# Optimization experiments

Hardware: AMD Instinct MI355X
Metric: run time of the kernel (lower is better)

## Reference

```python
import jax, jax.numpy as jnp
import numpy as np

B, S, E, H, NQ, FF = 4, 1024, 256, 32, 8, 1024
DK = E // H  # 8, equals n_wires of the quantum attention layer
EPS = 1e-5


def layernorm(x, g, b):
    mu = jnp.mean(x, axis=-1, keepdims=True)
    var = jnp.mean(jnp.square(x - mu), axis=-1, keepdims=True)
    return (x - mu) * jax.lax.rsqrt(var + EPS) * g + b


def setup_inputs() -> dict:
    key = jax.random.key(0)
    ks = jax.random.split(key, 20)
    s = lambda n: 1.0 / np.sqrt(n)
    return {
        "x": jax.random.normal(ks[0], (B, S, E), dtype=jnp.float32),
        # quantum attention trainable RX angles (one per wire)
        "theta_attn": jax.random.uniform(ks[1], (DK,), minval=-np.pi, maxval=np.pi),
        # nn.MultiheadAttention packed in-proj and out-proj
        "w_in": jax.random.normal(ks[2], (3 * E, E)) * s(E),
        "b_in": jnp.zeros((3 * E,), jnp.float32),
        "w_out": jax.random.normal(ks[3], (E, E)) * s(E),
        "b_out": jnp.zeros((E,), jnp.float32),
        # combine linear
        "w_comb": jax.random.normal(ks[4], (E, E)) * s(E),
        "b_comb": jnp.zeros((E,), jnp.float32),
        # layernorms
        "g1": jnp.ones((E,), jnp.float32), "be1": jnp.zeros((E,), jnp.float32),
        "g2": jnp.ones((E,), jnp.float32), "be2": jnp.zeros((E,), jnp.float32),
        # FFN: input_proj, quantum RY angles, linear1, linear2
        "w_ip": jax.random.normal(ks[5], (NQ, E)) * s(E),
        "b_ip": jnp.zeros((NQ,), jnp.float32),
        "theta_ffn": jax.random.uniform(ks[6], (NQ,), minval=-np.pi, maxval=np.pi),
        "w1": jax.random.normal(ks[7], (FF, NQ)) * s(NQ),
        "b1": jnp.zeros((FF,), jnp.float32),
        "w2": jax.random.normal(ks[8], (E, FF)) * s(FF),
        "b2": jnp.zeros((E,), jnp.float32),
    }


def reference(x, theta_attn, w_in, b_in, w_out, b_out, w_comb, b_comb,
              g1, be1, g2, be2, w_ip, b_ip, theta_ffn, w1, b1, w2, b2):
    batch, seq, embed = x.shape
    # ---- QuantumAttention ----
    # per-head RX(x_i) encoding followed by trainable RX(theta_i): <Z_i> = cos(x_i + theta_i)
    xh = x.reshape(batch, seq, H, DK)            # [B,S,H,dk]
    q_out = jnp.cos(xh + theta_attn).reshape(batch, seq, embed)
    # standard multi-head self-attention on q_out (q=k=v)
    qkv = q_out @ w_in.T + b_in                  # [B,S,3E]
    q, k, v = jnp.split(qkv, 3, axis=-1)
    def heads(t):
        return t.reshape(batch, seq, H, DK).transpose(0, 2, 1, 3)  # [B,H,S,dk]
    q, k, v = heads(q), heads(k), heads(v)
    scores = jnp.einsum('bhqd,bhkd->bhqk', q, k) / np.sqrt(DK)
    attn = jax.nn.softmax(scores, axis=-1)
    ctx = jnp.einsum('bhqk,bhkd->bhqd', attn, v)
    ctx = ctx.transpose(0, 2, 1, 3).reshape(batch, seq, embed)
    attn_out = (ctx @ w_out.T + b_out) @ w_comb.T + b_comb
    # ---- residual + norm1 ----
    h = layernorm(x + attn_out, g1, be1)
    # ---- QuantumFeedForward ----
    proj = h @ w_ip.T + b_ip                     # [B,S,NQ]
    # RX(x) encoding then trainable RY(phi): <Z> = cos(phi) * cos(x)
    qf = jnp.cos(theta_ffn) * jnp.cos(proj)
    ffn_out = jax.nn.relu(qf @ w1.T + b1) @ w2.T + b2
    # ---- residual + norm2 ----
    return layernorm(h + ffn_out, g2, be2)
```

## Files before the change

kernel.cpp:

```cpp
#include <hip/hip_runtime.h>
#include <hip/hip_bf16.h>

#define B_  4
#define S_  1024
#define E_  256
#define H_  32
#define NQ_ 8
#define FF_ 1024
#define M_  (B_*S_)
#define QS  0.5100880289202462f
#define VSTRIDE 1036

typedef __attribute__((ext_vector_type(8))) short bf16x8;
typedef __attribute__((ext_vector_type(4))) short short4v;
typedef __attribute__((ext_vector_type(4))) float f32x4;

#if __has_builtin(__builtin_amdgcn_exp2f)
#define EXP2 __builtin_amdgcn_exp2f
#else
#define EXP2 exp2f
#endif

__device__ inline short f2bf(float f) {
    union { float f; unsigned u; } v; v.f = f;
    unsigned r = (v.u + 0x7fff + ((v.u >> 16) & 1)) >> 16;
    return (short)r;
}

__device__ inline float bf2f(ushort u_) {
    union { unsigned u; float f; } c; c.u = ((unsigned)u_) << 16; return c.f;
}

__device__ inline unsigned pk2(float a, float b) {
    __hip_bfloat162 h = __float22bfloat162_rn(make_float2(a, b));
    union { __hip_bfloat162 h; unsigned u; } c; c.h = h;
    return c.u;
}

__global__ __launch_bounds__(256) void d1_kernel(
        const float* __restrict__ x, const float* __restrict__ theta_attn,
        const float* __restrict__ w_in, const float* __restrict__ b_in,
        const float* __restrict__ w_out, const float* __restrict__ w_comb,
        const float* __restrict__ b_out, const float* __restrict__ b_comb,
        const float* __restrict__ w2,
        ushort* __restrict__ qkv_bf, ushort* __restrict__ weff_bf,
        float* __restrict__ beff, ushort* __restrict__ w2_bf) {
    __shared__ ushort As[128 * 64];
    __shared__ ushort Bs[64 * 64];
    __shared__ float red[4];
    int bid = blockIdx.x, tid = threadIdx.x;

    if (bid >= 392) {
        if (bid < 648) {
            int i = bid - 392;
            float p = w_comb[(size_t)i * 256 + tid] * b_out[tid];
#pragma unroll
            for (int o = 32; o > 0; o >>= 1) p += __shfl_xor(p, o);
            if ((tid & 63) == 0) red[tid >> 6] = p;
            __syncthreads();
            if (tid == 0) beff[i] = red[0] + red[1] + red[2] + red[3] + b_comb[i];
        } else {
            int i = (bid - 648) * 256 + tid;
            float4 v = ((const float4*)w2)[i];
            short4v o = {f2bf(v.x), f2bf(v.y), f2bf(v.z), f2bf(v.w)};
            ((short4v*)w2_bf)[i] = o;
        }
        return;
    }

    bool isW = bid >= 384;
    int bm, bn;
    if (!isW) { bm = (bid / 12) * 128; bn = (bid % 12) * 64; }
    else      { int t = bid - 384; bm = (t >> 2) * 128; bn = (t & 3) * 64; }

    int w = tid >> 6, l = tid & 63, lq = l & 15, hi = l >> 4;
    int wm = w & 1, wn = w >> 1;
    f32x4 acc[4][2] = {};
    int srow = tid >> 3;
    int sk = (tid & 7) * 8;
    float wscale = isW ? 1.f : ((bn < 256) ? QS : 1.f);
    float th[8];
    if (!isW) {
#pragma unroll
        for (int j = 0; j < 8; ++j) th[j] = theta_attn[j];
    }

    for (int k0 = 0; k0 < 256; k0 += 64) {
        __syncthreads();
        if (!isW) {
#pragma unroll
            for (int it = 0; it < 4; ++it) {
                int row = it * 32 + srow;
                const float* xp = x + (size_t)(bm + row) * 256 + k0 + sk;
                float4 a = *(const float4*)xp;
                float4 b = *(const float4*)(xp + 4);
                bf16x8 o;
                o[0] = f2bf(__cosf(a.x + th[0]));
                o[1] = f2bf(__cosf(a.y + th[1]));
                o[2] = f2bf(__cosf(a.z + th[2]));
                o[3] = f2bf(__cosf(a.w + th[3]));
                o[4] = f2bf(__cosf(b.x + th[4]));
                o[5] = f2bf(__cosf(b.y + th[5]));
                o[6] = f2bf(__cosf(b.z + th[6]));
                o[7] = f2bf(__cosf(b.w + th[7]));
                *(bf16x8*)((char*)As + row * 128 + ((sk * 2) ^ ((row & 7) << 4))) = o;
            }
#pragma unroll
            for (int it = 0; it < 2; ++it) {
                int row = it * 32 + srow;
                const float* wp = w_in + (size_t)(bn + row) * 256 + k0 + sk;
                float4 a = *(const float4*)wp;
                float4 b = *(const float4*)(wp + 4);
                bf16x8 o;
                o[0] = f2bf(a.x * wscale); o[1] = f2bf(a.y * wscale);
                o[2] = f2bf(a.z * wscale); o[3] = f2bf(a.w * wscale);
                o[4] = f2bf(b.x * wscale); o[5] = f2bf(b.y * wscale);
                o[6] = f2bf(b.z * wscale); o[7] = f2bf(b.w * wscale);
                *(bf16x8*)((char*)Bs + row * 128 + ((sk * 2) ^ ((row & 7) << 4))) = o;
            }
        } else {
#pragma unroll
            for (int it = 0; it < 4; ++it) {
                int row = it * 32 + srow;
                const float* wp = w_comb + (size_t)(bm + row) * 256 + k0 + sk;
                float4 a = *(const float4*)wp;
                float4 b = *(const float4*)(wp + 4);
                bf16x8 o;
                o[0] = f2bf(a.x); o[1] = f2bf(a.y); o[2] = f2bf(a.z); o[3] = f2bf(a.w);
                o[4] = f2bf(b.x); o[5] = f2bf(b.y); o[6] = f2bf(b.z); o[7] = f2bf(b.w);
                *(bf16x8*)((char*)As + row * 128 + ((sk * 2) ^ ((row & 7) << 4))) = o;
            }
            int nl = tid & 63, kg = tid >> 6;
#pragma unroll
            for (int kk = 0; kk < 16; ++kk) {
                int kb = (kg * 16 + kk) * 2;
                float v = w_out[(size_t)(k0 + kg * 16 + kk) * 256 + bn + nl];
                *(ushort*)((char*)Bs + nl * 128 + (kb ^ ((nl & 7) << 4))) = (ushort)f2bf(v);
            }
        }
        __syncthreads();
#pragma unroll
        for (int kk = 0; kk < 2; ++kk) {
            bf16x8 af[4], bfr[2];
#pragma unroll
            for (int mf = 0; mf < 4; ++mf) {
                int row = wm * 64 + mf * 16 + lq;
                af[mf] = *(const bf16x8*)((const char*)As + row * 128 +
                                          ((kk * 64 + hi * 16) ^ ((row & 7) << 4)));
            }
#pragma unroll
            for (int nf = 0; nf < 2; ++nf) {
                int row = wn * 32 + nf * 16 + lq;
                bfr[nf] = *(const bf16x8*)((const char*)Bs + row * 128 +
                                           ((kk * 64 + hi * 16) ^ ((row & 7) << 4)));
            }
#pragma unroll
            for (int mf = 0; mf < 4; ++mf)
#pragma unroll
                for (int nf = 0; nf < 2; ++nf)
                    acc[mf][nf] = __builtin_amdgcn_mfma_f32_16x16x32_bf16(af[mf], bfr[nf], acc[mf][nf], 0, 0, 0);
        }
    }
    ushort* Cp = isW ? weff_bf : qkv_bf;
    int Nd = isW ? 256 : 768;
#pragma unroll
    for (int mf = 0; mf < 4; ++mf)
#pragma unroll
        for (int nf = 0; nf < 2; ++nf) {
            int n = bn + wn * 32 + nf * 16 + lq;
            float bv = isW ? 0.f : b_in[n] * wscale;
#pragma unroll
            for (int r = 0; r < 4; ++r) {
                int m = bm + wm * 64 + mf * 16 + hi * 4 + r;
                Cp[(size_t)m * Nd + n] = (ushort)f2bf(acc[mf][nf][r] + bv);
            }
        }
}

__global__ __launch_bounds__(256, 4) void attn_mfma_kernel(const ushort* __restrict__ qkv,
                                                           ushort* __restrict__ ctx) {
    __shared__ ushort vt[9 * VSTRIDE + 4];
    int qt = blockIdx.x, h = blockIdx.y, b = blockIdx.z;
    int tid = threadIdx.x;
    const ushort* base = qkv + (size_t)b * S_ * (3 * E_) + h * 8;

    for (int i = tid; i < S_; i += 256) {
        bf16x8 vv = *(const bf16x8*)(base + (size_t)i * (3 * E_) + 2 * E_);
        int kf = (i >> 4) & 3, hh = (i >> 2) & 3, s = i & 3;
        int pv = (i & ~63) + ((kf >> 1) << 5) + (hh << 3) + ((kf & 1) << 2) + s;
#pragma unroll
        for (int d = 0; d < 8; ++d) vt[d * VSTRIDE + pv] = vv[d];
        vt[8 * VSTRIDE + pv] = 0x3F80;
    }
    __syncthreads();

    int w = tid >> 6, l = tid & 63, lq = l & 15, g = l >> 4;

    bf16x8 qfrag[2];
#pragma unroll
    for (int qf = 0; qf < 2; ++qf) {
        bf16x8 qv = {};
        if (g == 0)
            qv = *(const bf16x8*)(base + (size_t)(qt * 128 + w * 32 + qf * 16 + lq) * (3 * E_));
        qfrag[qf] = qv;
    }

    f32x4 ctxa[2] = {{0.f,0.f,0.f,0.f},{0.f,0.f,0.f,0.f}};
    const f32x4 zf = {0.f, 0.f, 0.f, 0.f};

    for (int kt = 0; kt < 16; ++kt) {
        bf16x8 kfrag[4];
#pragma unroll
        for (int kf = 0; kf < 4; ++kf) {
            bf16x8 kv = {};
            if (g == 0)
                kv = *(const bf16x8*)(base + (size_t)(kt * 64 + kf * 16 + lq) * (3 * E_) + E_);
            kfrag[kf] = kv;
        }
        bf16x8 vf0 = *(bf16x8*)&vt[lq * VSTRIDE + kt * 64 + g * 8];
        bf16x8 vf1 = *(bf16x8*)&vt[lq * VSTRIDE + kt * 64 + 32 + g * 8];
#pragma unroll
        for (int qf = 0; qf < 2; ++qf) {
            f32x4 st[4];
#pragma unroll
            for (int kf = 0; kf < 4; ++kf)
                st[kf] = __builtin_amdgcn_mfma_f32_16x16x32_bf16(kfrag[kf], qfrag[qf], zf, 0, 0, 0);
            union { unsigned u[4]; bf16x8 v; } p0, p1;
            p0.u[0] = pk2(EXP2(st[0][0]), EXP2(st[0][1]));
            p0.u[1] = pk2(EXP2(st[0][2]), EXP2(st[0][3]));
            p0.u[2] = pk2(EXP2(st[1][0]), EXP2(st[1][1]));
            p0.u[3] = pk2(EXP2(st[1][2]), EXP2(st[1][3]));
            p1.u[0] = pk2(EXP2(st[2][0]), EXP2(st[2][1]));
            p1.u[1] = pk2(EXP2(st[2][2]), EXP2(st[2][3]));
            p1.u[2] = pk2(EXP2(st[3][0]), EXP2(st[3][1]));
            p1.u[3] = pk2(EXP2(st[3][2]), EXP2(st[3][3]));
            ctxa[qf] = __builtin_amdgcn_mfma_f32_16x16x32_bf16(p0.v, vf0, ctxa[qf], 0, 0, 0);
            ctxa[qf] = __builtin_amdgcn_mfma_f32_16x16x32_bf16(p1.v, vf1, ctxa[qf], 0, 0, 0);
        }
    }

#pragma unroll
    for (int qf = 0; qf < 2; ++qf) {
        int src = (l & 48) + 8;
        float s0 = __shfl(ctxa[qf][0], src);
        float s1 = __shfl(ctxa[qf][1], src);
        float s2 = __shfl(ctxa[qf][2], src);
        float s3 = __shfl(ctxa[qf][3], src);
        if (lq < 8) {
            int tok = b * S_ + qt * 128 + w * 32 + qf * 16 + g * 4;
            ushort* cp = ctx + (size_t)tok * E_ + h * 8 + lq;
            cp[0]      = (ushort)f2bf(ctxa[qf][0] / s0);
            cp[E_]     = (ushort)f2bf(ctxa[qf][1] / s1);
            cp[2 * E_] = (ushort)f2bf(ctxa[qf][2] / s2);
            cp[3 * E_] = (ushort)f2bf(ctxa[qf][3] / s3);
        }
    }
}

__global__ __launch_bounds__(512) void d3_kernel(
        const ushort* __restrict__ ctx, const ushort* __restrict__ weff,
        const float* __restrict__ beff, const float* __restrict__ x,
        const float* __restrict__ g1, const float* __restrict__ be1,
        const float* __restrict__ w_ip, const float* __restrict__ b_ip,
        const float* __restrict__ theta_ffn,
        const float* __restrict__ w1, const float* __restrict__ b1,
        float* __restrict__ h, ushort* __restrict__ t_bf) {
    __shared__ union {
        struct { ushort As[64 * 64]; ushort Bs[256 * 64]; } st;
        struct { ushort hl[64 * 264]; float qfl[64 * 9]; ushort w1l[8192]; } ph;
    } u;
    __shared__ float red[2][64][4];
    int tid = threadIdx.x;
    int bm = blockIdx.x * 64;
    int w = tid >> 6, l = tid & 63, lq = l & 15, hi = l >> 4;
    int wm = w >> 2, wn = w & 3;
    f32x4 acc[2][4] = {};
    int srow = tid >> 3, sk = (tid & 7) * 8;

    for (int k0 = 0; k0 < 256; k0 += 64) {
        __syncthreads();
        {
            bf16x8 v = *(const bf16x8*)(ctx + (size_t)(bm + srow) * 256 + k0 + sk);
            *(bf16x8*)((char*)u.st.As + srow * 128 + ((sk * 2) ^ ((srow & 7) << 4))) = v;
        }
#pragma unroll
        for (int it = 0; it < 4; ++it) {
            int v8 = it * 512 + tid;
            int row = v8 >> 3, kb = (v8 & 7) * 16;
            bf16x8 v = *(const bf16x8*)(weff + (size_t)row * 256 + k0 + (kb >> 1));
            *(bf16x8*)((char*)u.st.Bs + row * 128 + (kb ^ ((row & 7) << 4))) = v;
        }
        __syncthreads();
#pragma unroll
        for (int kk = 0; kk < 2; ++kk) {
            bf16x8 af[2], bfr[4];
#pragma unroll
            for (int mf = 0; mf < 2; ++mf) {
                int row = wm * 32 + mf * 16 + lq;
                af[mf] = *(const bf16x8*)((const char*)u.st.As + row * 128 +
                                          ((kk * 64 + hi * 16) ^ ((row & 7) << 4)));
            }
#pragma unroll
            for (int nf = 0; nf < 4; ++nf) {
                int row = wn * 64 + nf * 16 + lq;
                bfr[nf] = *(const bf16x8*)((const char*)u.st.Bs + row * 128 +
                                           ((kk * 64 + hi * 16) ^ ((row & 7) << 4)));
            }
#pragma unroll
            for (int mf = 0; mf < 2; ++mf)
#pragma unroll
                for (int nf = 0; nf < 4; ++nf)
                    acc[mf][nf] = __builtin_amdgcn_mfma_f32_16x16x32_bf16(af[mf], bfr[nf], acc[mf][nf], 0, 0, 0);
        }
    }
    __syncthreads();

    float bv[4];
#pragma unroll
    for (int nf = 0; nf < 4; ++nf) bv[nf] = beff[wn * 64 + nf * 16 + lq];
    float vv[2][4][4];
    float rs[2][4] = {}, rq[2][4] = {};
#pragma unroll
    for (int mf = 0; mf < 2; ++mf)
#pragma unroll
        for (int nf = 0; nf < 4; ++nf) {
            int n = wn * 64 + nf * 16 + lq;
#pragma unroll
            for (int r = 0; r < 4; ++r) {
                int m = bm + wm * 32 + mf * 16 + hi * 4 + r;
                float val = acc[mf][nf][r] + bv[nf] + x[(size_t)m * 256 + n];
                vv[mf][nf][r] = val;
                rs[mf][r] += val;
                rq[mf][r] += val * val;
            }
        }
#pragma unroll
    for (int o = 1; o < 16; o <<= 1)
#pragma unroll
        for (int mf = 0; mf < 2; ++mf)
#pragma unroll
            for (int r = 0; r < 4; ++r) {
                rs[mf][r] += __shfl_xor(rs[mf][r], o);
                rq[mf][r] += __shfl_xor(rq[mf][r], o);
            }
    if (lq == 0) {
#pragma unroll
        for (int mf = 0; mf < 2; ++mf)
#pragma unroll
            for (int r = 0; r < 4; ++r) {
                int row = wm * 32 + mf * 16 + hi * 4 + r;
                red[0][row][wn] = rs[mf][r];
                red[1][row][wn] = rq[mf][r];
            }
    }
    __syncthreads();
#pragma unroll
    for (int mf = 0; mf < 2; ++mf)
#pragma unroll
        for (int r = 0; r < 4; ++r) {
            int row = wm * 32 + mf * 16 + hi * 4 + r;
            float st_ = red[0][row][0] + red[0][row][1] + red[0][row][2] + red[0][row][3];
            float sq_ = red[1][row][0] + red[1][row][1] + red[1][row][2] + red[1][row][3];
            float mu = st_ * (1.f / 256.f);
            float var = sq_ * (1.f / 256.f) - mu * mu;
            rs[mf][r] = mu;
            rq[mf][r] = rsqrtf(var + 1e-5f);
        }
#pragma unroll
    for (int mf = 0; mf < 2; ++mf)
#pragma unroll
        for (int nf = 0; nf < 4; ++nf) {
            int n = wn * 64 + nf * 16 + lq;
            float gn = g1[n], bn_ = be1[n];
#pragma unroll
            for (int r = 0; r < 4; ++r) {
                int row = wm * 32 + mf * 16 + hi * 4 + r;
                float vn = (vv[mf][nf][r] - rs[mf][r]) * rq[mf][r] * gn + bn_;
                h[(size_t)(bm + row) * 256 + n] = vn;
                u.ph.hl[row * 264 + n] = (ushort)f2bf(vn);
            }
        }
    for (int i = tid; i < 8192; i += 512) u.ph.w1l[i] = (ushort)f2bf(w1[i]);
    __syncthreads();

    {
        int tok = tid >> 3, wq = tid & 7;
        const float* wip = w_ip + wq * 256;
        float pr = 0.f;
#pragma unroll
        for (int c = 0; c < 32; ++c) {
            bf16x8 hv = *(const bf16x8*)&u.ph.hl[tok * 264 + c * 8];
            float4 wa = *(const float4*)(wip + c * 8);
            float4 wb = *(const float4*)(wip + c * 8 + 4);
            pr += bf2f((ushort)hv[0]) * wa.x + bf2f((ushort)hv[1]) * wa.y
                + bf2f((ushort)hv[2]) * wa.z + bf2f((ushort)hv[3]) * wa.w
                + bf2f((ushort)hv[4]) * wb.x + bf2f((ushort)hv[5]) * wb.y
                + bf2f((ushort)hv[6]) * wb.z + bf2f((ushort)hv[7]) * wb.w;
        }
        u.ph.qfl[tok * 9 + wq] = __cosf(theta_ffn[wq]) * __cosf(pr + b_ip[wq]);
    }
    __syncthreads();

    for (int it = 0; it < 16; ++it) {
        int idx = it * 512 + tid;
        int tok = idx >> 7, fb = (idx & 127) * 8;
        float q[8];
#pragma unroll
        for (int j = 0; j < 8; ++j) q[j] = u.ph.qfl[tok * 9 + j];
        float4 ba = *(const float4*)(b1 + fb);
        float4 bb = *(const float4*)(b1 + fb + 4);
        float sa[8] = {ba.x, ba.y, ba.z, ba.w, bb.x, bb.y, bb.z, bb.w};
        bf16x8 o;
#pragma unroll
        for (int j = 0; j < 8; ++j) {
            bf16x8 wv = *(const bf16x8*)&u.ph.w1l[(fb + j) * 8];
            float s = sa[j];
#pragma unroll
            for (int k = 0; k < 8; ++k) s += q[k] * bf2f((ushort)wv[k]);
            o[j] = f2bf(fmaxf(s, 0.f));
        }
        *(bf16x8*)(t_bf + (size_t)(bm + tok) * 1024 + fb) = o;
    }
}

__global__ __launch_bounds__(512) void d4_kernel(
        const ushort* __restrict__ t_bf, const ushort* __restrict__ w2b,
        const float* __restrict__ b2, const float* __restrict__ h,
        const float* __restrict__ g2, const float* __restrict__ be2,
        float* __restrict__ out) {
    __shared__ ushort As[64 * 64];
    __shared__ ushort Bs[256 * 64];
    __shared__ float red[2][64][4];
    int tid = threadIdx.x;
    int bm = blockIdx.x * 64;
    int w = tid >> 6, l = tid & 63, lq = l & 15, hi = l >> 4;
    int wm = w >> 2, wn = w & 3;
    f32x4 acc[2][4] = {};
    int srow = tid >> 3, sk = (tid & 7) * 8;

    for (int k0 = 0; k0 < 1024; k0 += 64) {
        __syncthreads();
        {
            bf16x8 v = *(const bf16x8*)(t_bf + (size_t)(bm + srow) * 1024 + k0 + sk);
            *(bf16x8*)((char*)As + srow * 128 + ((sk * 2) ^ ((srow & 7) << 4))) = v;
        }
#pragma unroll
        for (int it = 0; it < 4; ++it) {
            int v8 = it * 512 + tid;
            int row = v8 >> 3, kb = (v8 & 7) * 16;
            bf16x8 v = *(const bf16x8*)(w2b + (size_t)row * 1024 + k0 + (kb >> 1));
            *(bf16x8*)((char*)Bs + row * 128 + (kb ^ ((row & 7) << 4))) = v;
        }
        __syncthreads();
#pragma unroll
        for (int kk = 0; kk < 2; ++kk) {
            bf16x8 af[2], bfr[4];
#pragma unroll
            for (int mf = 0; mf < 2; ++mf) {
                int row = wm * 32 + mf * 16 + lq;
                af[mf] = *(const bf16x8*)((const char*)As + row * 128 +
                                          ((kk * 64 + hi * 16) ^ ((row & 7) << 4)));
            }
#pragma unroll
            for (int nf = 0; nf < 4; ++nf) {
                int row = wn * 64 + nf * 16 + lq;
                bfr[nf] = *(const bf16x8*)((const char*)Bs + row * 128 +
                                           ((kk * 64 + hi * 16) ^ ((row & 7) << 4)));
            }
#pragma unroll
            for (int mf = 0; mf < 2; ++mf)
#pragma unroll
                for (int nf = 0; nf < 4; ++nf)
                    acc[mf][nf] = __builtin_amdgcn_mfma_f32_16x16x32_bf16(af[mf], bfr[nf], acc[mf][nf], 0, 0, 0);
        }
    }

    float bv[4];
#pragma unroll
    for (int nf = 0; nf < 4; ++nf) bv[nf] = b2[wn * 64 + nf * 16 + lq];
    float vv[2][4][4];
    float rs[2][4] = {}, rq[2][4] = {};
#pragma unroll
    for (int mf = 0; mf < 2; ++mf)
#pragma unroll
        for (int nf = 0; nf < 4; ++nf) {
            int n = wn * 64 + nf * 16 + lq;
#pragma unroll
            for (int r = 0; r < 4; ++r) {
                int m = bm + wm * 32 + mf * 16 + hi * 4 + r;
                float val = acc[mf][nf][r] + bv[nf] + h[(size_t)m * 256 + n];
                vv[mf][nf][r] = val;
                rs[mf][r] += val;
                rq[mf][r] += val * val;
            }
        }
#pragma unroll
    for (int o = 1; o < 16; o <<= 1)
#pragma unroll
        for (int mf = 0; mf < 2; ++mf)
#pragma unroll
            for (int r = 0; r < 4; ++r) {
                rs[mf][r] += __shfl_xor(rs[mf][r], o);
                rq[mf][r] += __shfl_xor(rq[mf][r], o);
            }
    if (lq == 0) {
#pragma unroll
        for (int mf = 0; mf < 2; ++mf)
#pragma unroll
            for (int r = 0; r < 4; ++r) {
                int row = wm * 32 + mf * 16 + hi * 4 + r;
                red[0][row][wn] = rs[mf][r];
                red[1][row][wn] = rq[mf][r];
            }
    }
    __syncthreads();
#pragma unroll
    for (int mf = 0; mf < 2; ++mf)
#pragma unroll
        for (int r = 0; r < 4; ++r) {
            int row = wm * 32 + mf * 16 + hi * 4 + r;
            float st_ = red[0][row][0] + red[0][row][1] + red[0][row][2] + red[0][row][3];
            float sq_ = red[1][row][0] + red[1][row][1] + red[1][row][2] + red[1][row][3];
            float mu = st_ * (1.f / 256.f);
            float var = sq_ * (1.f / 256.f) - mu * mu;
            rs[mf][r] = mu;
            rq[mf][r] = rsqrtf(var + 1e-5f);
        }
#pragma unroll
    for (int mf = 0; mf < 2; ++mf)
#pragma unroll
        for (int nf = 0; nf < 4; ++nf) {
            int n = wn * 64 + nf * 16 + lq;
            float gn = g2[n], bn_ = be2[n];
#pragma unroll
            for (int r = 0; r < 4; ++r) {
                int row = wm * 32 + mf * 16 + hi * 4 + r;
                out[(size_t)(bm + row) * 256 + n] =
                    (vv[mf][nf][r] - rs[mf][r]) * rq[mf][r] * gn + bn_;
            }
        }
}

extern "C" void kernel_launch(void* const* d_in, const int* in_sizes, int n_in,
                              void* d_out, int out_size, void* d_ws, size_t ws_size,
                              hipStream_t stream) {
    const float* x          = (const float*)d_in[0];
    const float* theta_attn = (const float*)d_in[1];
    const float* w_in       = (const float*)d_in[2];
    const float* b_in       = (const float*)d_in[3];
    const float* w_out      = (const float*)d_in[4];
    const float* b_out      = (const float*)d_in[5];
    const float* w_comb     = (const float*)d_in[6];
    const float* b_comb     = (const float*)d_in[7];
    const float* g1         = (const float*)d_in[8];
    const float* be1        = (const float*)d_in[9];
    const float* g2         = (const float*)d_in[10];
    const float* be2        = (const float*)d_in[11];
    const float* w_ip       = (const float*)d_in[12];
    const float* b_ip       = (const float*)d_in[13];
    const float* theta_ffn  = (const float*)d_in[14];
    const float* w1         = (const float*)d_in[15];
    const float* b1         = (const float*)d_in[16];
    const float* w2         = (const float*)d_in[17];
    const float* b2         = (const float*)d_in[18];
    float* out = (float*)d_out;

    char* wsb = (char*)d_ws;
    ushort* qkv_bf  = (ushort*)(wsb);
    ushort* ctx_bf  = (ushort*)(wsb + (6u << 20));
    ushort* t_bf    = (ushort*)(wsb + (8u << 20));
    float*  h       = (float*)(wsb + (16u << 20));
    ushort* weff_bf = (ushort*)(wsb + (20u << 20));
    ushort* w2_bf   = (ushort*)(wsb + (20u << 20) + 131072);
    float*  beff    = (float*)(wsb + (20u << 20) + 655360);

    d1_kernel<<<904, 256, 0, stream>>>(x, theta_attn, w_in, b_in, w_out, w_comb,
                                       b_out, b_comb, w2, qkv_bf, weff_bf, beff, w2_bf);
    attn_mfma_kernel<<<dim3(S_ / 128, H_, B_), 256, 0, stream>>>(qkv_bf, ctx_bf);
    d3_kernel<<<M_ / 64, 512, 0, stream>>>(ctx_bf, weff_bf, beff, x, g1, be1,
                                           w_ip, b_ip, theta_ffn, w1, b1, h, t_bf);
    d4_kernel<<<M_ / 64, 512, 0, stream>>>(t_bf, w2_bf, b2, h, g2, be2, out);
}
```

Before: 217.4 us.

## Recompute FFN hidden in d4 from qf, shrink row tiles, stage K in LDS

```diff
diff --git a/kernel.cpp b/kernel.cpp
--- a/kernel.cpp
+++ b/kernel.cpp
@@ -179,13 +179,17 @@
 
 __global__ __launch_bounds__(256, 4) void attn_mfma_kernel(const ushort* __restrict__ qkv,
                                                            ushort* __restrict__ ctx) {
+    __shared__ ushort ks[S_ * 8];
     __shared__ ushort vt[9 * VSTRIDE + 4];
     int qt = blockIdx.x, h = blockIdx.y, b = blockIdx.z;
     int tid = threadIdx.x;
     const ushort* base = qkv + (size_t)b * S_ * (3 * E_) + h * 8;
 
     for (int i = tid; i < S_; i += 256) {
-        bf16x8 vv = *(const bf16x8*)(base + (size_t)i * (3 * E_) + 2 * E_);
+        const ushort* rp = base + (size_t)i * (3 * E_);
+        bf16x8 kv = *(const bf16x8*)(rp + E_);
+        bf16x8 vv = *(const bf16x8*)(rp + 2 * E_);
+        *(bf16x8*)&ks[i * 8] = kv;
         int kf = (i >> 4) & 3, hh = (i >> 2) & 3, s = i & 3;
         int pv = (i & ~63) + ((kf >> 1) << 5) + (hh << 3) + ((kf & 1) << 2) + s;
 #pragma unroll
@@ -213,8 +217,7 @@
 #pragma unroll
         for (int kf = 0; kf < 4; ++kf) {
             bf16x8 kv = {};
-            if (g == 0)
-                kv = *(const bf16x8*)(base + (size_t)(kt * 64 + kf * 16 + lq) * (3 * E_) + E_);
+            if (g == 0) kv = *(bf16x8*)&ks[(kt * 64 + kf * 16 + lq) * 8];
             kfrag[kf] = kv;
         }
         bf16x8 vf0 = *(bf16x8*)&vt[lq * VSTRIDE + kt * 64 + g * 8];
@@ -257,35 +260,33 @@
     }
 }
 
-__global__ __launch_bounds__(512) void d3_kernel(
+__global__ __launch_bounds__(256) void d3_kernel(
         const ushort* __restrict__ ctx, const ushort* __restrict__ weff,
         const float* __restrict__ beff, const float* __restrict__ x,
         const float* __restrict__ g1, const float* __restrict__ be1,
         const float* __restrict__ w_ip, const float* __restrict__ b_ip,
         const float* __restrict__ theta_ffn,
-        const float* __restrict__ w1, const float* __restrict__ b1,
-        float* __restrict__ h, ushort* __restrict__ t_bf) {
+        float* __restrict__ h, float* __restrict__ qf) {
     __shared__ union {
-        struct { ushort As[64 * 64]; ushort Bs[256 * 64]; } st;
-        struct { ushort hl[64 * 264]; float qfl[64 * 9]; ushort w1l[8192]; } ph;
+        struct { ushort As[16 * 64]; ushort Bs[256 * 64]; } st;
+        ushort hl[16 * 264];
     } u;
-    __shared__ float red[2][64][4];
+    __shared__ float red[2][16][4];
     int tid = threadIdx.x;
-    int bm = blockIdx.x * 64;
-    int w = tid >> 6, l = tid & 63, lq = l & 15, hi = l >> 4;
-    int wm = w >> 2, wn = w & 3;
-    f32x4 acc[2][4] = {};
-    int srow = tid >> 3, sk = (tid & 7) * 8;
+    int bm = blockIdx.x * 16;
+    int wn = tid >> 6, l = tid & 63, lq = l & 15, hi = l >> 4;
+    f32x4 acc[4] = {};
 
     for (int k0 = 0; k0 < 256; k0 += 64) {
         __syncthreads();
-        {
-            bf16x8 v = *(const bf16x8*)(ctx + (size_t)(bm + srow) * 256 + k0 + sk);
-            *(bf16x8*)((char*)u.st.As + srow * 128 + ((sk * 2) ^ ((srow & 7) << 4))) = v;
-        }
-#pragma unroll
-        for (int it = 0; it < 4; ++it) {
-            int v8 = it * 512 + tid;
+        if (tid < 128) {
+            int row = tid >> 3, sk = (tid & 7) * 8;
+            bf16x8 v = *(const bf16x8*)(ctx + (size_t)(bm + row) * 256 + k0 + sk);
+            *(bf16x8*)((char*)u.st.As + row * 128 + ((sk * 2) ^ ((row & 7) << 4))) = v;
+        }
+#pragma unroll
+        for (int it = 0; it < 8; ++it) {
+            int v8 = it * 256 + tid;
             int row = v8 >> 3, kb = (v8 & 7) * 16;
             bf16x8 v = *(const bf16x8*)(weff + (size_t)row * 256 + k0 + (kb >> 1));
             *(bf16x8*)((char*)u.st.Bs + row * 128 + (kb ^ ((row & 7) << 4))) = v;
@@ -293,13 +294,9 @@
         __syncthreads();
 #pragma unroll
         for (int kk = 0; kk < 2; ++kk) {
-            bf16x8 af[2], bfr[4];
-#pragma unroll
-            for (int mf = 0; mf < 2; ++mf) {
-                int row = wm * 32 + mf * 16 + lq;
-                af[mf] = *(const bf16x8*)((const char*)u.st.As + row * 128 +
-                                          ((kk * 64 + hi * 16) ^ ((row & 7) << 4)));
-            }
+            bf16x8 af, bfr[4];
+            af = *(const bf16x8*)((const char*)u.st.As + lq * 128 +
+                                  ((kk * 64 + hi * 16) ^ ((lq & 7) << 4)));
 #pragma unroll
             for (int nf = 0; nf < 4; ++nf) {
                 int row = wn * 64 + nf * 16 + lq;
@@ -307,89 +304,74 @@
                                            ((kk * 64 + hi * 16) ^ ((row & 7) << 4)));
             }
 #pragma unroll
-            for (int mf = 0; mf < 2; ++mf)
-#pragma unroll
-                for (int nf = 0; nf < 4; ++nf)
-                    acc[mf][nf] = __builtin_amdgcn_mfma_f32_16x16x32_bf16(af[mf], bfr[nf], acc[mf][nf], 0, 0, 0);
-        }
-    }
-    __syncthreads();
-
-    float bv[4];
-#pragma unroll
-    for (int nf = 0; nf < 4; ++nf) bv[nf] = beff[wn * 64 + nf * 16 + lq];
-    float vv[2][4][4];
-    float rs[2][4] = {}, rq[2][4] = {};
-#pragma unroll
-    for (int mf = 0; mf < 2; ++mf)
-#pragma unroll
-        for (int nf = 0; nf < 4; ++nf) {
-            int n = wn * 64 + nf * 16 + lq;
-#pragma unroll
-            for (int r = 0; r < 4; ++r) {
-                int m = bm + wm * 32 + mf * 16 + hi * 4 + r;
-                float val = acc[mf][nf][r] + bv[nf] + x[(size_t)m * 256 + n];
-                vv[mf][nf][r] = val;
-                rs[mf][r] += val;
-                rq[mf][r] += val * val;
-            }
-        }
+            for (int nf = 0; nf < 4; ++nf)
+                acc[nf] = __builtin_amdgcn_mfma_f32_16x16x32_bf16(af, bfr[nf], acc[nf], 0, 0, 0);
+        }
+    }
+    __syncthreads();
+
+    float vv[4][4];
+    float rs[4] = {}, rq[4] = {};
+#pragma unroll
+    for (int nf = 0; nf < 4; ++nf) {
+        int n = wn * 64 + nf * 16 + lq;
+        float bv = beff[n];
+#pragma unroll
+        for (int r = 0; r < 4; ++r) {
+            int m = bm + hi * 4 + r;
+            float val = acc[nf][r] + bv + x[(size_t)m * 256 + n];
+            vv[nf][r] = val;
+            rs[r] += val;
+            rq[r] += val * val;
+        }
+    }
 #pragma unroll
     for (int o = 1; o < 16; o <<= 1)
 #pragma unroll
-        for (int mf = 0; mf < 2; ++mf)
-#pragma unroll
-            for (int r = 0; r < 4; ++r) {
-                rs[mf][r] += __shfl_xor(rs[mf][r], o);
-                rq[mf][r] += __shfl_xor(rq[mf][r], o);
-            }
+        for (int r = 0; r < 4; ++r) {
+            rs[r] += __shfl_xor(rs[r], o);
+            rq[r] += __shfl_xor(rq[r], o);
+        }
     if (lq == 0) {
 #pragma unroll
-        for (int mf = 0; mf < 2; ++mf)
-#pragma unroll
-            for (int r = 0; r < 4; ++r) {
-                int row = wm * 32 + mf * 16 + hi * 4 + r;
-                red[0][row][wn] = rs[mf][r];
-                red[1][row][wn] = rq[mf][r];
-            }
-    }
-    __syncthreads();
-#pragma unroll
-    for (int mf = 0; mf < 2; ++mf)
-#pragma unroll
-        for (int r = 0; r < 4; ++r) {
-            int row = wm * 32 + mf * 16 + hi * 4 + r;
-            float st_ = red[0][row][0] + red[0][row][1] + red[0][row][2] + red[0][row][3];
-            float sq_ = red[1][row][0] + red[1][row][1] + red[1][row][2] + red[1][row][3];
-            float mu = st_ * (1.f / 256.f);
-            float var = sq_ * (1.f / 256.f) - mu * mu;
-            rs[mf][r] = mu;
-            rq[mf][r] = rsqrtf(var + 1e-5f);
-        }
-#pragma unroll
-    for (int mf = 0; mf < 2; ++mf)
-#pragma unroll
-        for (int nf = 0; nf < 4; ++nf) {
-            int n = wn * 64 + nf * 16 + lq;
-            float gn = g1[n], bn_ = be1[n];
-#pragma unroll
-            for (int r = 0; r < 4; ++r) {
-                int row = wm * 32 + mf * 16 + hi * 4 + r;
-                float vn = (vv[mf][nf][r] - rs[mf][r]) * rq[mf][r] * gn + bn_;
-                h[(size_t)(bm + row) * 256 + n] = vn;
-                u.ph.hl[row * 264 + n] = (ushort)f2bf(vn);
-            }
-        }
-    for (int i = tid; i < 8192; i += 512) u.ph.w1l[i] = (ushort)f2bf(w1[i]);
-    __syncthreads();
-
-    {
+        for (int r = 0; r < 4; ++r) {
+            red[0][hi * 4 + r][wn] = rs[r];
+            red[1][hi * 4 + r][wn] = rq[r];
+        }
+    }
+    __syncthreads();
+#pragma unroll
+    for (int r = 0; r < 4; ++r) {
+        int row = hi * 4 + r;
+        float st_ = red[0][row][0] + red[0][row][1] + red[0][row][2] + red[0][row][3];
+        float sq_ = red[1][row][0] + red[1][row][1] + red[1][row][2] + red[1][row][3];
+        float mu = st_ * (1.f / 256.f);
+        float var = sq_ * (1.f / 256.f) - mu * mu;
+        rs[r] = mu;
+        rq[r] = rsqrtf(var + 1e-5f);
+    }
+    __syncthreads();
+#pragma unroll
+    for (int nf = 0; nf < 4; ++nf) {
+        int n = wn * 64 + nf * 16 + lq;
+        float gn = g1[n], bn_ = be1[n];
+#pragma unroll
+        for (int r = 0; r < 4; ++r) {
+            int row = hi * 4 + r;
+            float vn = (vv[nf][r] - rs[r]) * rq[r] * gn + bn_;
+            h[(size_t)(bm + row) * 256 + n] = vn;
+            u.hl[row * 264 + n] = (ushort)f2bf(vn);
+        }
+    }
+    __syncthreads();
+
+    if (tid < 128) {
         int tok = tid >> 3, wq = tid & 7;
         const float* wip = w_ip + wq * 256;
         float pr = 0.f;
 #pragma unroll
         for (int c = 0; c < 32; ++c) {
-            bf16x8 hv = *(const bf16x8*)&u.ph.hl[tok * 264 + c * 8];
+            bf16x8 hv = *(const bf16x8*)&u.hl[tok * 264 + c * 8];
             float4 wa = *(const float4*)(wip + c * 8);
             float4 wb = *(const float4*)(wip + c * 8 + 4);
             pr += bf2f((ushort)hv[0]) * wa.x + bf2f((ushort)hv[1]) * wa.y
@@ -397,56 +379,57 @@
                 + bf2f((ushort)hv[4]) * wb.x + bf2f((ushort)hv[5]) * wb.y
                 + bf2f((ushort)hv[6]) * wb.z + bf2f((ushort)hv[7]) * wb.w;
         }
-        u.ph.qfl[tok * 9 + wq] = __cosf(theta_ffn[wq]) * __cosf(pr + b_ip[wq]);
-    }
-    __syncthreads();
-
-    for (int it = 0; it < 16; ++it) {
-        int idx = it * 512 + tid;
-        int tok = idx >> 7, fb = (idx & 127) * 8;
-        float q[8];
-#pragma unroll
-        for (int j = 0; j < 8; ++j) q[j] = u.ph.qfl[tok * 9 + j];
-        float4 ba = *(const float4*)(b1 + fb);
-        float4 bb = *(const float4*)(b1 + fb + 4);
-        float sa[8] = {ba.x, ba.y, ba.z, ba.w, bb.x, bb.y, bb.z, bb.w};
-        bf16x8 o;
-#pragma unroll
-        for (int j = 0; j < 8; ++j) {
-            bf16x8 wv = *(const bf16x8*)&u.ph.w1l[(fb + j) * 8];
-            float s = sa[j];
-#pragma unroll
-            for (int k = 0; k < 8; ++k) s += q[k] * bf2f((ushort)wv[k]);
-            o[j] = f2bf(fmaxf(s, 0.f));
-        }
-        *(bf16x8*)(t_bf + (size_t)(bm + tok) * 1024 + fb) = o;
-    }
-}
-
-__global__ __launch_bounds__(512) void d4_kernel(
-        const ushort* __restrict__ t_bf, const ushort* __restrict__ w2b,
+        qf[(size_t)(bm + tok) * NQ_ + wq] = __cosf(theta_ffn[wq]) * __cosf(pr + b_ip[wq]);
+    }
+}
+
+__global__ __launch_bounds__(256) void d4_kernel(
+        const float* __restrict__ qf, const float* __restrict__ w1,
+        const float* __restrict__ b1, const ushort* __restrict__ w2b,
         const float* __restrict__ b2, const float* __restrict__ h,
         const float* __restrict__ g2, const float* __restrict__ be2,
         float* __restrict__ out) {
-    __shared__ ushort As[64 * 64];
+    __shared__ ushort As[16 * 64];
     __shared__ ushort Bs[256 * 64];
-    __shared__ float red[2][64][4];
+    __shared__ ushort w1l[FF_ * 8];
+    __shared__ float b1l[FF_];
+    __shared__ float qfl[16 * 8];
+    __shared__ float red[2][16][4];
     int tid = threadIdx.x;
-    int bm = blockIdx.x * 64;
-    int w = tid >> 6, l = tid & 63, lq = l & 15, hi = l >> 4;
-    int wm = w >> 2, wn = w & 3;
-    f32x4 acc[2][4] = {};
-    int srow = tid >> 3, sk = (tid & 7) * 8;
+    int bm = blockIdx.x * 16;
+    int wn = tid >> 6, l = tid & 63, lq = l & 15, hi = l >> 4;
+    f32x4 acc[4] = {};
+
+#pragma unroll
+    for (int it = 0; it < 32; ++it) w1l[it * 256 + tid] = (ushort)f2bf(w1[it * 256 + tid]);
+#pragma unroll
+    for (int it = 0; it < 4; ++it) b1l[it * 256 + tid] = b1[it * 256 + tid];
+    if (tid < 128) qfl[tid] = qf[(size_t)bm * NQ_ + tid];
+    __syncthreads();
 
     for (int k0 = 0; k0 < 1024; k0 += 64) {
         __syncthreads();
-        {
-            bf16x8 v = *(const bf16x8*)(t_bf + (size_t)(bm + srow) * 1024 + k0 + sk);
-            *(bf16x8*)((char*)As + srow * 128 + ((sk * 2) ^ ((srow & 7) << 4))) = v;
-        }
-#pragma unroll
-        for (int it = 0; it < 4; ++it) {
-            int v8 = it * 512 + tid;
+        if (tid < 128) {
+            int row = tid >> 3, j8 = tid & 7;
+            int f0 = k0 + j8 * 8;
+            float q[8];
+#pragma unroll
+            for (int k = 0; k < 8; ++k) q[k] = qfl[row * 8 + k];
+            bf16x8 o;
+#pragma unroll
+            for (int j = 0; j < 8; ++j) {
+                bf16x8 wv = *(const bf16x8*)&w1l[(f0 + j) * 8];
+                float s = b1l[f0 + j];
+#pragma unroll
+                for (int k = 0; k < 8; ++k) s += q[k] * bf2f((ushort)wv[k]);
+                o[j] = f2bf(fmaxf(s, 0.f));
+            }
+            int sk = j8 * 8;
+            *(bf16x8*)((char*)As + row * 128 + ((sk * 2) ^ ((row & 7) << 4))) = o;
+        }
+#pragma unroll
+        for (int it = 0; it < 8; ++it) {
+            int v8 = it * 256 + tid;
             int row = v8 >> 3, kb = (v8 & 7) * 16;
             bf16x8 v = *(const bf16x8*)(w2b + (size_t)row * 1024 + k0 + (kb >> 1));
             *(bf16x8*)((char*)Bs + row * 128 + (kb ^ ((row & 7) << 4))) = v;
@@ -454,13 +437,9 @@
         __syncthreads();
 #pragma unroll
         for (int kk = 0; kk < 2; ++kk) {
-            bf16x8 af[2], bfr[4];
-#pragma unroll
-            for (int mf = 0; mf < 2; ++mf) {
-                int row = wm * 32 + mf * 16 + lq;
-                af[mf] = *(const bf16x8*)((const char*)As + row * 128 +
-                                          ((kk * 64 + hi * 16) ^ ((row & 7) << 4)));
-            }
+            bf16x8 af, bfr[4];
+            af = *(const bf16x8*)((const char*)As + lq * 128 +
+                                  ((kk * 64 + hi * 16) ^ ((lq & 7) << 4)));
 #pragma unroll
             for (int nf = 0; nf < 4; ++nf) {
                 int row = wn * 64 + nf * 16 + lq;
@@ -468,77 +447,62 @@
                                            ((kk * 64 + hi * 16) ^ ((row & 7) << 4)));
             }
 #pragma unroll
-            for (int mf = 0; mf < 2; ++mf)
-#pragma unroll
-                for (int nf = 0; nf < 4; ++nf)
-                    acc[mf][nf] = __builtin_amdgcn_mfma_f32_16x16x32_bf16(af[mf], bfr[nf], acc[mf][nf], 0, 0, 0);
-        }
-    }
-
-    float bv[4];
-#pragma unroll
-    for (int nf = 0; nf < 4; ++nf) bv[nf] = b2[wn * 64 + nf * 16 + lq];
-    float vv[2][4][4];
-    float rs[2][4] = {}, rq[2][4] = {};
-#pragma unroll
-    for (int mf = 0; mf < 2; ++mf)
-#pragma unroll
-        for (int nf = 0; nf < 4; ++nf) {
-            int n = wn * 64 + nf * 16 + lq;
-#pragma unroll
-            for (int r = 0; r < 4; ++r) {
-                int m = bm + wm * 32 + mf * 16 + hi * 4 + r;
-                float val = acc[mf][nf][r] + bv[nf] + h[(size_t)m * 256 + n];
-                vv[mf][nf][r] = val;
-                rs[mf][r] += val;
-                rq[mf][r] += val * val;
-            }
-        }
+            for (int nf = 0; nf < 4; ++nf)
+                acc[nf] = __builtin_amdgcn_mfma_f32_16x16x32_bf16(af, bfr[nf], acc[nf], 0, 0, 0);
+        }
+    }
+
+    float vv[4][4];
+    float rs[4] = {}, rq[4] = {};
+#pragma unroll
+    for (int nf = 0; nf < 4; ++nf) {
+        int n = wn * 64 + nf * 16 + lq;
+        float bv = b2[n];
+#pragma unroll
+        for (int r = 0; r < 4; ++r) {
+            int m = bm + hi * 4 + r;
+            float val = acc[nf][r] + bv + h[(size_t)m * 256 + n];
+            vv[nf][r] = val;
+            rs[r] += val;
+            rq[r] += val * val;
+        }
+    }
 #pragma unroll
     for (int o = 1; o < 16; o <<= 1)
 #pragma unroll
-        for (int mf = 0; mf < 2; ++mf)
-#pragma unroll
-            for (int r = 0; r < 4; ++r) {
-                rs[mf][r] += __shfl_xor(rs[mf][r], o);
-                rq[mf][r] += __shfl_xor(rq[mf][r], o);
-            }
+        for (int r = 0; r < 4; ++r) {
+            rs[r] += __shfl_xor(rs[r], o);
+            rq[r] += __shfl_xor(rq[r], o);
+        }
     if (lq == 0) {
 #pragma unroll
-        for (int mf = 0; mf < 2; ++mf)
-#pragma unroll
-            for (int r = 0; r < 4; ++r) {
-                int row = wm * 32 + mf * 16 + hi * 4 + r;
-                red[0][row][wn] = rs[mf][r];
-                red[1][row][wn] = rq[mf][r];
-            }
-    }
-    __syncthreads();
-#pragma unroll
-    for (int mf = 0; mf < 2; ++mf)
-#pragma unroll
-        for (int r = 0; r < 4; ++r) {
-            int row = wm * 32 + mf * 16 + hi * 4 + r;
-            float st_ = red[0][row][0] + red[0][row][1] + red[0][row][2] + red[0][row][3];
-            float sq_ = red[1][row][0] + red[1][row][1] + red[1][row][2] + red[1][row][3];
-            float mu = st_ * (1.f / 256.f);
-            float var = sq_ * (1.f / 256.f) - mu * mu;
-            rs[mf][r] = mu;
-            rq[mf][r] = rsqrtf(var + 1e-5f);
-        }
-#pragma unroll
-    for (int mf = 0; mf < 2; ++mf)
-#pragma unroll
-        for (int nf = 0; nf < 4; ++nf) {
-            int n = wn * 64 + nf * 16 + lq;
-            float gn = g2[n], bn_ = be2[n];
-#pragma unroll
-            for (int r = 0; r < 4; ++r) {
-                int row = wm * 32 + mf * 16 + hi * 4 + r;
-                out[(size_t)(bm + row) * 256 + n] =
-                    (vv[mf][nf][r] - rs[mf][r]) * rq[mf][r] * gn + bn_;
-            }
-        }
+        for (int r = 0; r < 4; ++r) {
+            red[0][hi * 4 + r][wn] = rs[r];
+            red[1][hi * 4 + r][wn] = rq[r];
+        }
+    }
+    __syncthreads();
+#pragma unroll
+    for (int r = 0; r < 4; ++r) {
+        int row = hi * 4 + r;
+        float st_ = red[0][row][0] + red[0][row][1] + red[0][row][2] + red[0][row][3];
+        float sq_ = red[1][row][0] + red[1][row][1] + red[1][row][2] + red[1][row][3];
+        float mu = st_ * (1.f / 256.f);
+        float var = sq_ * (1.f / 256.f) - mu * mu;
+        rs[r] = mu;
+        rq[r] = rsqrtf(var + 1e-5f);
+    }
+#pragma unroll
+    for (int nf = 0; nf < 4; ++nf) {
+        int n = wn * 64 + nf * 16 + lq;
+        float gn = g2[n], bn_ = be2[n];
+#pragma unroll
+        for (int r = 0; r < 4; ++r) {
+            int row = hi * 4 + r;
+            out[(size_t)(bm + row) * 256 + n] =
+                (vv[nf][r] - rs[r]) * rq[r] * gn + bn_;
+        }
+    }
 }
 
 extern "C" void kernel_launch(void* const* d_in, const int* in_sizes, int n_in,
@@ -568,16 +532,16 @@
     char* wsb = (char*)d_ws;
     ushort* qkv_bf  = (ushort*)(wsb);
     ushort* ctx_bf  = (ushort*)(wsb + (6u << 20));
-    ushort* t_bf    = (ushort*)(wsb + (8u << 20));
-    float*  h       = (float*)(wsb + (16u << 20));
-    ushort* weff_bf = (ushort*)(wsb + (20u << 20));
-    ushort* w2_bf   = (ushort*)(wsb + (20u << 20) + 131072);
-    float*  beff    = (float*)(wsb + (20u << 20) + 655360);
+    float*  h       = (float*)(wsb + (8u << 20));
+    float*  qf      = (float*)(wsb + (12u << 20));
+    ushort* weff_bf = (ushort*)(wsb + (13u << 20));
+    ushort* w2_bf   = (ushort*)(wsb + (13u << 20) + 131072);
+    float*  beff    = (float*)(wsb + (14u << 20));
 
     d1_kernel<<<904, 256, 0, stream>>>(x, theta_attn, w_in, b_in, w_out, w_comb,
                                        b_out, b_comb, w2, qkv_bf, weff_bf, beff, w2_bf);
     attn_mfma_kernel<<<dim3(S_ / 128, H_, B_), 256, 0, stream>>>(qkv_bf, ctx_bf);
-    d3_kernel<<<M_ / 64, 512, 0, stream>>>(ctx_bf, weff_bf, beff, x, g1, be1,
-                                           w_ip, b_ip, theta_ffn, w1, b1, h, t_bf);
-    d4_kernel<<<M_ / 64, 512, 0, stream>>>(t_bf, w2_bf, b2, h, g2, be2, out);
-}
+    d3_kernel<<<M_ / 16, 256, 0, stream>>>(ctx_bf, weff_bf, beff, x, g1, be1,
+                                           w_ip, b_ip, theta_ffn, h, qf);
+    d4_kernel<<<M_ / 16, 256, 0, stream>>>(qf, w1, b1, w2_bf, b2, h, g2, be2, out);
+}
```

Measured after the change: 183.0 us. 15.8% less time.
